# Optimization experiments

Hardware: AMD Instinct MI355X
Metric: run time of the kernel (lower is better)

The kernel has to match this reference:

```python
import jax, jax.numpy as jnp
import numpy as np

PADDING = 1
STRIDE = 1

def setup_inputs() -> dict:
    key = jax.random.key(0)
    k1, k2 = jax.random.split(key)
    x = jax.random.normal(k1, (32, 64, 64, 64), dtype=jnp.float32)
    # kaiming_normal fan_out, relu: std = sqrt(2 / (out_ch * k * k))
    fan_out = 128 * 3 * 3
    std = np.sqrt(2.0 / fan_out).astype(np.float32)
    weight = jax.random.normal(k2, (128, 64, 3, 3), dtype=jnp.float32) * std
    bias = jnp.zeros((128,), dtype=jnp.float32)
    return {"x": x, "weight": weight, "bias": bias}

def reference(x, weight, bias):
    # Faithful to the unfold+multiply+sum path, which computes a standard
    # cross-correlation conv2d (torch conv semantics) with stride/padding.
    out = jax.lax.conv_general_dilated(
        x, weight,
        window_strides=(STRIDE, STRIDE),
        padding=[(PADDING, PADDING), (PADDING, PADDING)],
        dimension_numbers=("NCHW", "OIHW", "NCHW"),
    )
    return out + bias[None, :, None, None]
```

## Files before the change

### kernel.cpp

```cpp
#include <hip/hip_runtime.h>


typedef short short8 __attribute__((ext_vector_type(8)));
typedef float f32x4  __attribute__((ext_vector_type(4)));

static __device__ __forceinline__ unsigned short f2bf(float f) {
    unsigned int u = __float_as_uint(f);
    u = (u + 0x7FFFu + ((u >> 16) & 1u)) >> 16;
    return (unsigned short)u;
}
static __device__ __forceinline__ unsigned int pk2(float lo, float hi) {
    return (unsigned int)f2bf(lo) | ((unsigned int)f2bf(hi) << 16);
}

__global__ __launch_bounds__(256)
void prep_x(const float* __restrict__ x, unsigned short* __restrict__ xT)
{
    __shared__ float T[64][65];
    const int h = blockIdx.x, n = blockIdx.y, tid = threadIdx.x;
    const size_t nbase = (size_t)n * 262144 + (size_t)h * 64;
    #pragma unroll
    for (int i = 0; i < 16; ++i) {
        int idx = tid + i * 256;
        int ci = idx >> 6, w = idx & 63;
        T[ci][w] = x[nbase + (size_t)ci * 4096 + w];
    }
    __syncthreads();
    const int w = tid >> 2, cg = tid & 3;
    unsigned int pk[8];
    #pragma unroll
    for (int k = 0; k < 8; ++k)
        pk[k] = pk2(T[cg * 16 + 2 * k][w], T[cg * 16 + 2 * k + 1][w]);
    unsigned short* dst = xT + (((size_t)n * 64 + h) * 64 + w) * 64 + cg * 16;
    uint4 a; a.x = pk[0]; a.y = pk[1]; a.z = pk[2]; a.w = pk[3];
    uint4 b; b.x = pk[4]; b.y = pk[5]; b.z = pk[6]; b.w = pk[7];
    *(uint4*)(dst)     = a;
    *(uint4*)(dst + 8) = b;
}

__global__ __launch_bounds__(256)
void prep_w(const float* __restrict__ w, unsigned short* __restrict__ wT)
{
    int t = blockIdx.x * 256 + threadIdx.x;
    if (t >= 128 * 576) return;
    int co = t / 576, r = t - co * 576;
    int p = r >> 6, ci = r & 63;
    wT[t] = f2bf(w[(size_t)(co * 64 + ci) * 9 + p]);
}

#define XLDS_BYTES 84480
#define WLDS_BYTES 16384
#define TOTAL_LDS  (XLDS_BYTES + 2 * WLDS_BYTES)

__global__ __launch_bounds__(512, 2)
void conv_mfma(const unsigned short* __restrict__ xT,
               const unsigned short* __restrict__ wT,
               const float* __restrict__ bias,
               float* __restrict__ out)
{
    extern __shared__ __align__(16) char lds[];
    char* Wl = lds + XLDS_BYTES;

    const int tid = threadIdx.x;
    const int h0  = blockIdx.x * 8;
    const int n   = blockIdx.y;
    const int wid = tid >> 6, lane = tid & 63;
    const int wm = wid >> 2, wn = wid & 3;
    const int l15 = lane & 15, l4 = lane >> 4;

    {
        const unsigned short* xTn = xT + (size_t)n * 262144;
        for (int G = tid; G < 5280; G += 512) {
            int hp = G / 528;
            int r  = G - hp * 528;
            int wp = r >> 3, g = r & 7;
            int gh = h0 + hp - 1, gw = wp - 1;
            uint4 v; v.x = v.y = v.z = v.w = 0u;
            if ((unsigned)gh < 64u && (unsigned)gw < 64u)
                v = *(const uint4*)(xTn + ((gh * 64 + gw) * 64 + g * 8));
            *(uint4*)(lds + ((hp * 66 + wp) * 64 + ((g ^ (wp & 7)) * 8)) * 2) = v;
        }
    }

    const int wco0 = tid >> 3, wg = tid & 7;
    const int wds0 = (wco0 * 64 + ((wg ^ (wco0 & 7)) * 8)) * 2;
    const int wds1 = ((wco0 + 64) * 64 + ((wg ^ ((wco0 + 64) & 7)) * 8)) * 2;
    const unsigned short* wsrc0 = wT + wco0 * 576 + wg * 8;
    const unsigned short* wsrc1 = wT + (wco0 + 64) * 576 + wg * 8;

    {
        uint4 a = *(const uint4*)(wsrc0);
        uint4 b = *(const uint4*)(wsrc1);
        *(uint4*)(Wl + wds0) = a;
        *(uint4*)(Wl + wds1) = b;
    }
    __syncthreads();

    f32x4 acc[4][8];
    #pragma unroll
    for (int mf = 0; mf < 4; ++mf)
        #pragma unroll
        for (int nf = 0; nf < 8; ++nf)
            acc[mf][nf] = (f32x4)0.0f;

    #pragma unroll
    for (int p = 0; p < 9; ++p) {
        const int kh = p / 3, kw = p - kh * 3;
        const int bufoff = (p & 1) * WLDS_BYTES;

        uint4 nw0, nw1;
        if (p < 8) {
            nw0 = *(const uint4*)(wsrc0 + (p + 1) * 64);
            nw1 = *(const uint4*)(wsrc1 + (p + 1) * 64);
        }

        #pragma unroll
        for (int ci0 = 0; ci0 < 64; ci0 += 32) {
            const int cg = ci0 >> 3;
            short8 Af[4], Bf[8];
            #pragma unroll
            for (int mf = 0; mf < 4; ++mf) {
                const int co = wm * 64 + mf * 16 + l15;
                const int g  = (cg + l4) ^ (co & 7);
                Af[mf] = *(const short8*)(Wl + bufoff + co * 128 + g * 16);
            }
            #pragma unroll
            for (int nf = 0; nf < 8; ++nf) {
                const int hp = wn * 2 + (nf >> 2) + kh;
                const int wp = (nf & 3) * 16 + l15 + kw;
                const int g  = (cg + l4) ^ (wp & 7);
                Bf[nf] = *(const short8*)(lds + (hp * 66 + wp) * 128 + g * 16);
            }
            #pragma unroll
            for (int mf = 0; mf < 4; ++mf)
                #pragma unroll
                for (int nf = 0; nf < 8; ++nf)
                    acc[mf][nf] = __builtin_amdgcn_mfma_f32_16x16x32_bf16(
                        Af[mf], Bf[nf], acc[mf][nf], 0, 0, 0);
        }

        if (p < 8) {
            *(uint4*)(Wl + (bufoff ^ WLDS_BYTES) + wds0) = nw0;
            *(uint4*)(Wl + (bufoff ^ WLDS_BYTES) + wds1) = nw1;
        }
        __syncthreads();
    }

    #pragma unroll
    for (int mf = 0; mf < 4; ++mf) {
        #pragma unroll
        for (int reg = 0; reg < 4; ++reg) {
            const int co = wm * 64 + mf * 16 + l4 * 4 + reg;
            const float bv = bias[co];
            #pragma unroll
            for (int nf = 0; nf < 8; ++nf) {
                const int s = wn * 128 + nf * 16 + l15;
                const int h = h0 + (s >> 6);
                const int w = s & 63;
                out[(((size_t)n * 128 + co) * 64 + h) * 64 + w] = acc[mf][nf][reg] + bv;
            }
        }
    }
}

__global__ __launch_bounds__(256, 4)
void conv2d_f32_tiled(const float* __restrict__ x,
                      const float* __restrict__ wgt,
                      const float* __restrict__ bias,
                      float* __restrict__ out)
{
    __shared__ float Xlds[8][10][66];
    __shared__ float Wlds[32][72];
    const int tid = threadIdx.x;
    const int co0 = blockIdx.x * 32, h0 = blockIdx.y * 8, n = blockIdx.z;
    const int tco = tid >> 6, lane = tid & 63;
    float acc[8][8];
    #pragma unroll
    for (int i = 0; i < 8; ++i)
        #pragma unroll
        for (int j = 0; j < 8; ++j) acc[i][j] = 0.0f;
    for (int cc = 0; cc < 8; ++cc) {
        const int ci0 = cc * 8;
        for (int idx = tid; idx < 8 * 10 * 66; idx += 256) {
            const int ww = idx % 66, t = idx / 66, hh = t % 10, ci = t / 10;
            const int gh = h0 + hh - 1, gw = ww - 1;
            float v = 0.0f;
            if ((unsigned)gh < 64u && (unsigned)gw < 64u)
                v = x[(((size_t)n * 64 + ci0 + ci) * 64 + gh) * 64 + gw];
            Xlds[ci][hh][ww] = v;
        }
        for (int idx = tid; idx < 32 * 72; idx += 256) {
            const int r = idx % 72, co = idx / 72;
            Wlds[co][r] = wgt[(size_t)(co0 + co) * 576 + ci0 * 9 + r];
        }
        __syncthreads();
        for (int ci = 0; ci < 8; ++ci)
            #pragma unroll
            for (int kh = 0; kh < 3; ++kh)
                #pragma unroll
                for (int kw = 0; kw < 3; ++kw) {
                    float wv[8];
                    #pragma unroll
                    for (int i = 0; i < 8; ++i) wv[i] = Wlds[tco * 8 + i][ci * 9 + kh * 3 + kw];
                    #pragma unroll
                    for (int j = 0; j < 8; ++j) {
                        const float xv = Xlds[ci][j + kh][lane + kw];
                        #pragma unroll
                        for (int i = 0; i < 8; ++i) acc[i][j] = fmaf(wv[i], xv, acc[i][j]);
                    }
                }
        __syncthreads();
    }
    #pragma unroll
    for (int i = 0; i < 8; ++i) {
        const int co = co0 + tco * 8 + i;
        const float b = bias[co];
        #pragma unroll
        for (int j = 0; j < 8; ++j)
            out[(((size_t)n * 128 + co) * 64 + (h0 + j)) * 64 + lane] = acc[i][j] + b;
    }
}

extern "C" void kernel_launch(void* const* d_in, const int* in_sizes, int n_in,
                              void* d_out, int out_size, void* d_ws, size_t ws_size,
                              hipStream_t stream)
{
    const float* x    = (const float*)d_in[0];
    const float* wgt  = (const float*)d_in[1];
    const float* bias = (const float*)d_in[2];
    float* out        = (float*)d_out;

    const size_t XT_BYTES = (size_t)32 * 64 * 64 * 64 * 2;
    const size_t WT_BYTES = (size_t)128 * 576 * 2;

    if (ws_size < XT_BYTES + WT_BYTES) {
        dim3 grid(4, 8, 32);
        conv2d_f32_tiled<<<grid, 256, 0, stream>>>(x, wgt, bias, out);
        return;
    }

    unsigned short* xT = (unsigned short*)d_ws;
    unsigned short* wT = (unsigned short*)((char*)d_ws + XT_BYTES);

    (void)hipFuncSetAttribute((const void*)conv_mfma,
                              hipFuncAttributeMaxDynamicSharedMemorySize, TOTAL_LDS);

    prep_x<<<dim3(64, 32), 256, 0, stream>>>(x, xT);
    prep_w<<<dim3((128 * 576 + 255) / 256), 256, 0, stream>>>(wgt, wT);
    conv_mfma<<<dim3(8, 32), 512, TOTAL_LDS, stream>>>(xT, wT, bias, out);
}
```

Measured before the change: 44.03 us.

## Split conv tile into two half-row passes with prefetched input and register-held weights

```diff
diff --git a/kernel.cpp b/kernel.cpp
--- a/kernel.cpp
+++ b/kernel.cpp
@@ -48,116 +48,165 @@
     wT[t] = f2bf(w[(size_t)(co * 64 + ci) * 9 + p]);
 }
 
-#define XLDS_BYTES 84480
-#define WLDS_BYTES 16384
-#define TOTAL_LDS  (XLDS_BYTES + 2 * WLDS_BYTES)
+#define XBUF 50688
+#define WBUF 16384
+#define TOTAL_LDS (2*XBUF + 2*WBUF)
 
 __global__ __launch_bounds__(512, 2)
-void conv_mfma(const unsigned short* __restrict__ xT,
-               const unsigned short* __restrict__ wT,
-               const float* __restrict__ bias,
-               float* __restrict__ out)
+void conv_mfma2(const unsigned short* __restrict__ xT,
+                const unsigned short* __restrict__ wT,
+                const float* __restrict__ bias,
+                float* __restrict__ out)
 {
     extern __shared__ __align__(16) char lds[];
-    char* Wl = lds + XLDS_BYTES;
-
-    const int tid = threadIdx.x;
-    const int h0  = blockIdx.x * 8;
-    const int n   = blockIdx.y;
-    const int wid = tid >> 6, lane = tid & 63;
-    const int wm = wid >> 2, wn = wid & 3;
-    const int l15 = lane & 15, l4 = lane >> 4;
+    char* wl = lds + 2 * XBUF;
+
+    const int tid  = threadIdx.x;
+    const int h0   = blockIdx.x * 8;
+    const int n    = blockIdx.y;
+    const int wid  = tid >> 6, lane = tid & 63;
+    const int wm   = wid >> 2;
+    const int wrow = wid & 3;
+    const int l15  = lane & 15, l4 = lane >> 4;
+
+    const unsigned short* xTn = xT + (size_t)n * 262144;
+
+    const int co0 = tid >> 3, wg = tid & 7;
+    uint4 wreg[18];
+    #pragma unroll
+    for (int p = 0; p < 9; ++p) {
+        wreg[p*2]   = *(const uint4*)(wT + ( co0       * 576 + p*64 + wg*8));
+        wreg[p*2+1] = *(const uint4*)(wT + ((co0 + 64) * 576 + p*64 + wg*8));
+    }
+    const int wds0 = co0*128 + ((wg ^ (co0 & 7)) * 16);
+    const int wds1 = wds0 + 64*128;
+
+    f32x4 breg[4];
+    #pragma unroll
+    for (int mf = 0; mf < 4; ++mf)
+        breg[mf] = *(const f32x4*)(bias + wm*64 + mf*16 + l4*4);
 
     {
-        const unsigned short* xTn = xT + (size_t)n * 262144;
-        for (int G = tid; G < 5280; G += 512) {
-            int hp = G / 528;
-            int r  = G - hp * 528;
-            int wp = r >> 3, g = r & 7;
-            int gh = h0 + hp - 1, gw = wp - 1;
-            uint4 v; v.x = v.y = v.z = v.w = 0u;
-            if ((unsigned)gh < 64u && (unsigned)gw < 64u)
-                v = *(const uint4*)(xTn + ((gh * 64 + gw) * 64 + g * 8));
-            *(uint4*)(lds + ((hp * 66 + wp) * 64 + ((g ^ (wp & 7)) * 8)) * 2) = v;
-        }
-    }
-
-    const int wco0 = tid >> 3, wg = tid & 7;
-    const int wds0 = (wco0 * 64 + ((wg ^ (wco0 & 7)) * 8)) * 2;
-    const int wds1 = ((wco0 + 64) * 64 + ((wg ^ ((wco0 + 64) & 7)) * 8)) * 2;
-    const unsigned short* wsrc0 = wT + wco0 * 576 + wg * 8;
-    const unsigned short* wsrc1 = wT + (wco0 + 64) * 576 + wg * 8;
-
-    {
-        uint4 a = *(const uint4*)(wsrc0);
-        uint4 b = *(const uint4*)(wsrc1);
-        *(uint4*)(Wl + wds0) = a;
-        *(uint4*)(Wl + wds1) = b;
-    }
+        uint4 xreg[7];
+        #pragma unroll
+        for (int k = 0; k < 7; ++k) {
+            int gran = tid + k*512;
+            if (k < 6 || tid < 96) {
+                int hp = gran / 528, rem = gran - hp*528;
+                int wp = rem >> 3, g = rem & 7;
+                int gh = h0 + hp - 1, gw = wp - 1;
+                uint4 v; v.x = v.y = v.z = v.w = 0u;
+                if ((unsigned)gh < 64u && (unsigned)gw < 64u)
+                    v = *(const uint4*)(xTn + ((gh*64 + gw)*64 + g*8));
+                xreg[k] = v;
+            }
+        }
+        #pragma unroll
+        for (int k = 0; k < 7; ++k) {
+            int gran = tid + k*512;
+            if (k < 6 || tid < 96) {
+                int hp = gran / 528, rem = gran - hp*528;
+                int wp = rem >> 3, g = rem & 7;
+                *(uint4*)(lds + (hp*66 + wp)*128 + ((g ^ (wp & 7)) * 16)) = xreg[k];
+            }
+        }
+    }
+    *(uint4*)(wl + wds0) = wreg[0];
+    *(uint4*)(wl + wds1) = wreg[1];
     __syncthreads();
 
-    f32x4 acc[4][8];
-    #pragma unroll
-    for (int mf = 0; mf < 4; ++mf)
-        #pragma unroll
-        for (int nf = 0; nf < 8; ++nf)
-            acc[mf][nf] = (f32x4)0.0f;
-
-    #pragma unroll
-    for (int p = 0; p < 9; ++p) {
-        const int kh = p / 3, kw = p - kh * 3;
-        const int bufoff = (p & 1) * WLDS_BYTES;
-
-        uint4 nw0, nw1;
-        if (p < 8) {
-            nw0 = *(const uint4*)(wsrc0 + (p + 1) * 64);
-            nw1 = *(const uint4*)(wsrc1 + (p + 1) * 64);
-        }
-
-        #pragma unroll
-        for (int ci0 = 0; ci0 < 64; ci0 += 32) {
-            const int cg = ci0 >> 3;
-            short8 Af[4], Bf[8];
+    for (int it = 0; it < 2; ++it) {
+        const char* xb = lds + it * XBUF;
+        f32x4 acc[4][4];
+        #pragma unroll
+        for (int mf = 0; mf < 4; ++mf)
             #pragma unroll
-            for (int mf = 0; mf < 4; ++mf) {
-                const int co = wm * 64 + mf * 16 + l15;
-                const int g  = (cg + l4) ^ (co & 7);
-                Af[mf] = *(const short8*)(Wl + bufoff + co * 128 + g * 16);
-            }
+            for (int nf = 0; nf < 4; ++nf)
+                acc[mf][nf] = (f32x4)0.0f;
+
+        uint4 xreg[7];
+
+        #pragma unroll
+        for (int p = 0; p < 9; ++p) {
+            const int gp = it*9 + p;
+            const char* wbr = wl + ((gp & 1) ? WBUF : 0);
+            char*       wbw = wl + ((gp & 1) ? 0 : WBUF);
+            const int kh = p / 3, kw = p - kh*3;
+
             #pragma unroll
-            for (int nf = 0; nf < 8; ++nf) {
-                const int hp = wn * 2 + (nf >> 2) + kh;
-                const int wp = (nf & 3) * 16 + l15 + kw;
-                const int g  = (cg + l4) ^ (wp & 7);
-                Bf[nf] = *(const short8*)(lds + (hp * 66 + wp) * 128 + g * 16);
-            }
-            #pragma unroll
-            for (int mf = 0; mf < 4; ++mf)
-                #pragma unroll
-                for (int nf = 0; nf < 8; ++nf)
-                    acc[mf][nf] = __builtin_amdgcn_mfma_f32_16x16x32_bf16(
-                        Af[mf], Bf[nf], acc[mf][nf], 0, 0, 0);
-        }
-
-        if (p < 8) {
-            *(uint4*)(Wl + (bufoff ^ WLDS_BYTES) + wds0) = nw0;
-            *(uint4*)(Wl + (bufoff ^ WLDS_BYTES) + wds1) = nw1;
-        }
-        __syncthreads();
-    }
-
-    #pragma unroll
-    for (int mf = 0; mf < 4; ++mf) {
-        #pragma unroll
-        for (int reg = 0; reg < 4; ++reg) {
-            const int co = wm * 64 + mf * 16 + l4 * 4 + reg;
-            const float bv = bias[co];
-            #pragma unroll
-            for (int nf = 0; nf < 8; ++nf) {
-                const int s = wn * 128 + nf * 16 + l15;
-                const int h = h0 + (s >> 6);
-                const int w = s & 63;
-                out[(((size_t)n * 128 + co) * 64 + h) * 64 + w] = acc[mf][nf][reg] + bv;
+            for (int c = 0; c < 2; ++c) {
+                short8 Af[4], Bf[4];
+                #pragma unroll
+                for (int mf = 0; mf < 4; ++mf) {
+                    const int co = wm*64 + mf*16 + l15;
+                    Af[mf] = *(const short8*)(wbr + co*128 + (((c*4 + l4) ^ (co & 7)) * 16));
+                }
+                #pragma unroll
+                for (int nf = 0; nf < 4; ++nf) {
+                    const int hp = wrow + kh;
+                    const int wp = nf*16 + l15 + kw;
+                    Bf[nf] = *(const short8*)(xb + (hp*66 + wp)*128 + (((c*4 + l4) ^ (wp & 7)) * 16));
+                }
+                #pragma unroll
+                for (int mf = 0; mf < 4; ++mf)
+                    #pragma unroll
+                    for (int nf = 0; nf < 4; ++nf)
+                        acc[mf][nf] = __builtin_amdgcn_mfma_f32_16x16x32_bf16(
+                            Af[mf], Bf[nf], acc[mf][nf], 0, 0, 0);
+            }
+
+            if (it == 0 && p == 6) {
+                #pragma unroll
+                for (int k = 0; k < 7; ++k) {
+                    int gran = tid + k*512;
+                    if (k < 6 || tid < 96) {
+                        int hp = gran / 528, rem = gran - hp*528;
+                        int wp = rem >> 3, g = rem & 7;
+                        int gh = h0 + 4 + hp - 1, gw = wp - 1;
+                        uint4 v; v.x = v.y = v.z = v.w = 0u;
+                        if ((unsigned)gh < 64u && (unsigned)gw < 64u)
+                            v = *(const uint4*)(xTn + ((gh*64 + gw)*64 + g*8));
+                        xreg[k] = v;
+                    }
+                }
+            }
+
+            if (p == 8) {
+                const int h = h0 + it*4 + wrow;
+                #pragma unroll
+                for (int mf = 0; mf < 4; ++mf) {
+                    #pragma unroll
+                    for (int r = 0; r < 4; ++r) {
+                        const int co = wm*64 + mf*16 + l4*4 + r;
+                        float* orow = out + (((size_t)n*128 + co)*64 + h)*64;
+                        const float bv = breg[mf][r];
+                        #pragma unroll
+                        for (int nf = 0; nf < 4; ++nf)
+                            orow[nf*16 + l15] = acc[mf][nf][r] + bv;
+                    }
+                }
+            }
+
+            if (it == 0 && p == 8) {
+                #pragma unroll
+                for (int k = 0; k < 7; ++k) {
+                    int gran = tid + k*512;
+                    if (k < 6 || tid < 96) {
+                        int hp = gran / 528, rem = gran - hp*528;
+                        int wp = rem >> 3, g = rem & 7;
+                        *(uint4*)(lds + XBUF + (hp*66 + wp)*128 + ((g ^ (wp & 7)) * 16)) = xreg[k];
+                    }
+                }
+            }
+
+            if (gp < 17) {
+                const int pn = (p == 8) ? 0 : (p + 1);
+                *(uint4*)(wbw + wds0) = wreg[pn*2];
+                *(uint4*)(wbw + wds1) = wreg[pn*2 + 1];
+                __builtin_amdgcn_sched_barrier(0);
+                asm volatile("s_waitcnt lgkmcnt(0)" ::: "memory");
+                __builtin_amdgcn_s_barrier();
+                __builtin_amdgcn_sched_barrier(0);
             }
         }
     }
@@ -242,10 +291,10 @@
     unsigned short* xT = (unsigned short*)d_ws;
     unsigned short* wT = (unsigned short*)((char*)d_ws + XT_BYTES);
 
-    (void)hipFuncSetAttribute((const void*)conv_mfma,
+    (void)hipFuncSetAttribute((const void*)conv_mfma2,
                               hipFuncAttributeMaxDynamicSharedMemorySize, TOTAL_LDS);
 
     prep_x<<<dim3(64, 32), 256, 0, stream>>>(x, xT);
     prep_w<<<dim3((128 * 576 + 255) / 256), 256, 0, stream>>>(wgt, wT);
-    conv_mfma<<<dim3(8, 32), 512, TOTAL_LDS, stream>>>(xT, wT, bias, out);
-}
+    conv_mfma2<<<dim3(8, 32), 512, TOTAL_LDS, stream>>>(xT, wT, bias, out);
+}
```

Result: slower. 56.36 us (+28.0%).

## Retile MFMA conv into smaller blocks split over output channels and rows

Applied to the files above, without the earlier changes.

```diff
diff --git a/kernel.cpp b/kernel.cpp
--- a/kernel.cpp
+++ b/kernel.cpp
@@ -48,65 +48,84 @@
     wT[t] = f2bf(w[(size_t)(co * 64 + ci) * 9 + p]);
 }
 
-#define XLDS_BYTES 84480
-#define WLDS_BYTES 16384
-#define TOTAL_LDS  (XLDS_BYTES + 2 * WLDS_BYTES)
-
-__global__ __launch_bounds__(512, 2)
-void conv_mfma(const unsigned short* __restrict__ xT,
-               const unsigned short* __restrict__ wT,
-               const float* __restrict__ bias,
-               float* __restrict__ out)
+#define XBUF 50688
+#define WBUF 8192
+#define TOTAL_LDS (XBUF + 2*WBUF)
+
+__global__ __launch_bounds__(256, 2)
+void conv_mfma3(const unsigned short* __restrict__ xT,
+                const unsigned short* __restrict__ wT,
+                const float* __restrict__ bias,
+                float* __restrict__ out)
 {
     extern __shared__ __align__(16) char lds[];
-    char* Wl = lds + XLDS_BYTES;
-
-    const int tid = threadIdx.x;
-    const int h0  = blockIdx.x * 8;
-    const int n   = blockIdx.y;
-    const int wid = tid >> 6, lane = tid & 63;
-    const int wm = wid >> 2, wn = wid & 3;
-    const int l15 = lane & 15, l4 = lane >> 4;
+    char* wl = lds + XBUF;
+
+    const int tid  = threadIdx.x;
+    const int cb   = blockIdx.x;
+    const int h0   = blockIdx.y * 4;
+    const int n    = blockIdx.z;
+    const int wrow = tid >> 6;
+    const int lane = tid & 63;
+    const int l15  = lane & 15, l4 = lane >> 4;
+
+    const unsigned short* xTn = xT + (size_t)n * 262144;
+    const unsigned short* wTb = wT + (size_t)cb * 64 * 576;
+
+    const int wco = tid >> 3, wg = tid & 7;
+    const int wds0 = wco * 128 + ((wg ^ (wco & 7)) * 16);
+    const int wds1 = wds0 + 32 * 128;
+    const unsigned short* wsrc0 = wTb + wco * 576 + wg * 8;
+    const unsigned short* wsrc1 = wTb + (wco + 32) * 576 + wg * 8;
+
+    f32x4 breg[4];
+    #pragma unroll
+    for (int mf = 0; mf < 4; ++mf)
+        breg[mf] = *(const f32x4*)(bias + cb * 64 + mf * 16 + l4 * 4);
 
     {
-        const unsigned short* xTn = xT + (size_t)n * 262144;
-        for (int G = tid; G < 5280; G += 512) {
-            int hp = G / 528;
-            int r  = G - hp * 528;
-            int wp = r >> 3, g = r & 7;
-            int gh = h0 + hp - 1, gw = wp - 1;
-            uint4 v; v.x = v.y = v.z = v.w = 0u;
-            if ((unsigned)gh < 64u && (unsigned)gw < 64u)
-                v = *(const uint4*)(xTn + ((gh * 64 + gw) * 64 + g * 8));
-            *(uint4*)(lds + ((hp * 66 + wp) * 64 + ((g ^ (wp & 7)) * 8)) * 2) = v;
-        }
-    }
-
-    const int wco0 = tid >> 3, wg = tid & 7;
-    const int wds0 = (wco0 * 64 + ((wg ^ (wco0 & 7)) * 8)) * 2;
-    const int wds1 = ((wco0 + 64) * 64 + ((wg ^ ((wco0 + 64) & 7)) * 8)) * 2;
-    const unsigned short* wsrc0 = wT + wco0 * 576 + wg * 8;
-    const unsigned short* wsrc1 = wT + (wco0 + 64) * 576 + wg * 8;
-
-    {
-        uint4 a = *(const uint4*)(wsrc0);
-        uint4 b = *(const uint4*)(wsrc1);
-        *(uint4*)(Wl + wds0) = a;
-        *(uint4*)(Wl + wds1) = b;
+        uint4 xreg[13];
+        #pragma unroll
+        for (int k = 0; k < 13; ++k) {
+            int G = tid + k * 256;
+            if (k < 12 || tid < 96) {
+                int hp = G / 528, rem = G - hp * 528;
+                int wp = rem >> 3, g = rem & 7;
+                int gh = h0 + hp - 1, gw = wp - 1;
+                uint4 v; v.x = v.y = v.z = v.w = 0u;
+                if ((unsigned)gh < 64u && (unsigned)gw < 64u)
+                    v = *(const uint4*)(xTn + ((gh * 64 + gw) * 64 + g * 8));
+                xreg[k] = v;
+            }
+        }
+        uint4 w0a = *(const uint4*)(wsrc0);
+        uint4 w0b = *(const uint4*)(wsrc1);
+        #pragma unroll
+        for (int k = 0; k < 13; ++k) {
+            int G = tid + k * 256;
+            if (k < 12 || tid < 96) {
+                int hp = G / 528, rem = G - hp * 528;
+                int wp = rem >> 3, g = rem & 7;
+                *(uint4*)(lds + (hp * 66 + wp) * 128 + ((g ^ (wp & 7)) * 16)) = xreg[k];
+            }
+        }
+        *(uint4*)(wl + wds0) = w0a;
+        *(uint4*)(wl + wds1) = w0b;
     }
     __syncthreads();
 
-    f32x4 acc[4][8];
+    f32x4 acc[4][4];
     #pragma unroll
     for (int mf = 0; mf < 4; ++mf)
         #pragma unroll
-        for (int nf = 0; nf < 8; ++nf)
+        for (int nf = 0; nf < 4; ++nf)
             acc[mf][nf] = (f32x4)0.0f;
 
     #pragma unroll
     for (int p = 0; p < 9; ++p) {
+        const char* wbr = wl + ((p & 1) ? WBUF : 0);
+        char*       wbw = wl + ((p & 1) ? 0 : WBUF);
         const int kh = p / 3, kw = p - kh * 3;
-        const int bufoff = (p & 1) * WLDS_BYTES;
 
         uint4 nw0, nw1;
         if (p < 8) {
@@ -115,49 +134,46 @@
         }
 
         #pragma unroll
-        for (int ci0 = 0; ci0 < 64; ci0 += 32) {
-            const int cg = ci0 >> 3;
-            short8 Af[4], Bf[8];
+        for (int c = 0; c < 2; ++c) {
+            short8 Af[4], Bf[4];
             #pragma unroll
             for (int mf = 0; mf < 4; ++mf) {
-                const int co = wm * 64 + mf * 16 + l15;
-                const int g  = (cg + l4) ^ (co & 7);
-                Af[mf] = *(const short8*)(Wl + bufoff + co * 128 + g * 16);
-            }
-            #pragma unroll
-            for (int nf = 0; nf < 8; ++nf) {
-                const int hp = wn * 2 + (nf >> 2) + kh;
-                const int wp = (nf & 3) * 16 + l15 + kw;
-                const int g  = (cg + l4) ^ (wp & 7);
-                Bf[nf] = *(const short8*)(lds + (hp * 66 + wp) * 128 + g * 16);
+                const int co = mf * 16 + l15;
+                Af[mf] = *(const short8*)(wbr + co * 128 + (((c * 4 + l4) ^ (co & 7)) * 16));
+            }
+            #pragma unroll
+            for (int nf = 0; nf < 4; ++nf) {
+                const int hp = wrow + kh;
+                const int wp = nf * 16 + l15 + kw;
+                Bf[nf] = *(const short8*)(lds + (hp * 66 + wp) * 128 + (((c * 4 + l4) ^ (wp & 7)) * 16));
             }
             #pragma unroll
             for (int mf = 0; mf < 4; ++mf)
                 #pragma unroll
-                for (int nf = 0; nf < 8; ++nf)
+                for (int nf = 0; nf < 4; ++nf)
                     acc[mf][nf] = __builtin_amdgcn_mfma_f32_16x16x32_bf16(
                         Af[mf], Bf[nf], acc[mf][nf], 0, 0, 0);
         }
 
         if (p < 8) {
-            *(uint4*)(Wl + (bufoff ^ WLDS_BYTES) + wds0) = nw0;
-            *(uint4*)(Wl + (bufoff ^ WLDS_BYTES) + wds1) = nw1;
-        }
-        __syncthreads();
-    }
-
-    #pragma unroll
-    for (int mf = 0; mf < 4; ++mf) {
-        #pragma unroll
-        for (int reg = 0; reg < 4; ++reg) {
-            const int co = wm * 64 + mf * 16 + l4 * 4 + reg;
-            const float bv = bias[co];
-            #pragma unroll
-            for (int nf = 0; nf < 8; ++nf) {
-                const int s = wn * 128 + nf * 16 + l15;
-                const int h = h0 + (s >> 6);
-                const int w = s & 63;
-                out[(((size_t)n * 128 + co) * 64 + h) * 64 + w] = acc[mf][nf][reg] + bv;
+            *(uint4*)(wbw + wds0) = nw0;
+            *(uint4*)(wbw + wds1) = nw1;
+            __syncthreads();
+        }
+    }
+
+    {
+        const int h = h0 + wrow;
+        #pragma unroll
+        for (int mf = 0; mf < 4; ++mf) {
+            #pragma unroll
+            for (int r = 0; r < 4; ++r) {
+                const int co = cb * 64 + mf * 16 + l4 * 4 + r;
+                float* orow = out + (((size_t)n * 128 + co) * 64 + h) * 64;
+                const float bv = breg[mf][r];
+                #pragma unroll
+                for (int nf = 0; nf < 4; ++nf)
+                    orow[nf * 16 + l15] = acc[mf][nf][r] + bv;
             }
         }
     }
@@ -242,10 +258,10 @@
     unsigned short* xT = (unsigned short*)d_ws;
     unsigned short* wT = (unsigned short*)((char*)d_ws + XT_BYTES);
 
-    (void)hipFuncSetAttribute((const void*)conv_mfma,
+    (void)hipFuncSetAttribute((const void*)conv_mfma3,
                               hipFuncAttributeMaxDynamicSharedMemorySize, TOTAL_LDS);
 
     prep_x<<<dim3(64, 32), 256, 0, stream>>>(x, xT);
     prep_w<<<dim3((128 * 576 + 255) / 256), 256, 0, stream>>>(wgt, wT);
-    conv_mfma<<<dim3(8, 32), 512, TOTAL_LDS, stream>>>(xT, wT, bias, out);
-}
+    conv_mfma3<<<dim3(2, 16, 32), 256, TOTAL_LDS, stream>>>(xT, wT, bias, out);
+}
```

After: 44.73 us. No clear change (+1.6%).
